# Performance work log

Measured on AMD Instinct MI355X. Metric: run time of the kernel, lower is better.

The kernel has to match this reference:

```python
import jax, jax.numpy as jnp
import numpy as np

LR = 0.1  # inner-loop learning rate from `param - 0.1 * grad`

D = 4096          # memory width d; key/val are (1, d) per docstring
CTX = 512         # loss_context_size: number of keys per update step


def setup_inputs() -> dict:
    key = jax.random.key(0)
    k1, k2, k3 = jax.random.split(key, 3)
    W = jax.random.normal(k1, (D, D), dtype=jnp.float32) / np.sqrt(D)
    keys = jax.random.normal(k2, (CTX, D), dtype=jnp.float32)
    vals = jax.random.normal(k3, (CTX, D), dtype=jnp.float32)
    return {"W": W, "keys": keys, "vals": vals}


def reference(W, keys, vals):
    # OneStep.forward: preds_i = functional_forward(key_i, (W,)) = key_i @ W,
    # loss = MSE(preds, vals); new_W = W - 0.1 * dloss/dW.
    # The per-key loop is batched into a single (CTX, D) x (D, D) matmul.
    def loss_fn(Wp):
        preds = keys @ Wp  # (CTX, D)
        return jnp.mean((preds - vals) ** 2)

    g = jax.grad(loss_fn)(W)
    return W - LR * g
```

## Files before the change

### kernel.cpp

```cpp
#include <hip/hip_runtime.h>
#include <hip/hip_bf16.h>


typedef __bf16 bf16_t;
typedef __bf16 bf16x8 __attribute__((ext_vector_type(8)));
typedef float f32x4 __attribute__((ext_vector_type(4)));

#define D_DIM 4096
#define CTX_N 512
#define UPD_SCALE 9.5367431640625e-8f

__device__ __forceinline__ void gld16(const bf16_t* g, bf16_t* l) {
    __builtin_amdgcn_global_load_lds(
        (const __attribute__((address_space(1))) void*)g,
        (__attribute__((address_space(3))) void*)l, 16, 0, 0);
}

__device__ __forceinline__ void t_body2(
    float* tile, const float* __restrict__ src, bf16_t* __restrict__ dstT,
    bf16_t* __restrict__ dstN, int M, int N, int bx, int by)
{
    const int tid = threadIdx.x;
    const int C0 = bx * 64, R0 = by * 64;
    const int r  = tid >> 2, cs = (tid & 3) * 16;

    const float* s = src + (size_t)(R0 + r) * N + C0 + cs;
    float f[16];
#pragma unroll
    for (int u = 0; u < 4; ++u) {
        const float4 v = ((const float4*)s)[u];
        f[4 * u + 0] = v.x; f[4 * u + 1] = v.y; f[4 * u + 2] = v.z; f[4 * u + 3] = v.w;
    }
#pragma unroll
    for (int u = 0; u < 16; ++u) tile[r * 65 + cs + u] = f[u];

    if (dstN) {
        bf16x8 v0, v1;
#pragma unroll
        for (int u = 0; u < 8; ++u) { v0[u] = (bf16_t)f[u]; v1[u] = (bf16_t)f[8 + u]; }
        bf16_t* d = dstN + (size_t)(R0 + r) * N + C0 + cs;
        *(bf16x8*)d = v0; *(bf16x8*)(d + 8) = v1;
    }
    __syncthreads();

    bf16x8 o0, o1;
#pragma unroll
    for (int u = 0; u < 8; ++u) {
        o0[u] = (bf16_t)tile[(cs + u) * 65 + r];
        o1[u] = (bf16_t)tile[(cs + 8 + u) * 65 + r];
    }
    bf16_t* d = dstT + (size_t)(C0 + r) * M + R0 + cs;
    *(bf16x8*)d = o0; *(bf16x8*)(d + 8) = o1;
}

__global__ __launch_bounds__(256) void t_all(
    const float* __restrict__ W, const float* __restrict__ K,
    const float* __restrict__ V, bf16_t* __restrict__ Wt,
    bf16_t* __restrict__ Kt, bf16_t* __restrict__ Kb, bf16_t* __restrict__ Vt)
{
    __shared__ float tile[64 * 65];
    const int y = blockIdx.y;
    if (y < 64)      t_body2(tile, W, Wt, nullptr, D_DIM, D_DIM, blockIdx.x, y);
    else if (y < 72) t_body2(tile, K, Kt, Kb,      CTX_N, D_DIM, blockIdx.x, y - 64);
    else             t_body2(tile, V, Vt, nullptr, CTX_N, D_DIM, blockIdx.x, y - 72);
}



__global__ __launch_bounds__(256, 2) void k1_residual(
    const bf16_t* __restrict__ Wt, const bf16_t* __restrict__ Kb,
    const bf16_t* __restrict__ Vt, bf16_t* __restrict__ Rt)
{
    __shared__ __align__(16) bf16_t stg[16384];

    const int tid = threadIdx.x, wave = tid >> 6, lane = tid & 63;
    const int j0 = blockIdx.x * 64, c0 = blockIdx.y * 64;
    const int l15 = lane & 15, quad = lane >> 4;
    const int wm = wave >> 1, wn = wave & 1;

    f32x4 acc[2][2] = {};

    const int rl = lane >> 3;
    const int sl = ((lane & 7) ^ rl) * 8;
    const bf16_t* gA0 = Wt + (size_t)(j0 + wave * 8      + rl) * D_DIM + sl;
    const bf16_t* gA1 = Wt + (size_t)(j0 + wave * 8 + 32 + rl) * D_DIM + sl;
    const bf16_t* gB0 = Kb + (size_t)(c0 + wave * 8      + rl) * D_DIM + sl;
    const bf16_t* gB1 = Kb + (size_t)(c0 + wave * 8 + 32 + rl) * D_DIM + sl;

    auto stage = [&](int bsel, int t) {
        bf16_t* buf = stg + bsel * 8192;
        gld16(gA0 + t * 64, buf + (size_t)wave * 512 + lane * 8);
        gld16(gA1 + t * 64, buf + (size_t)(wave + 4) * 512 + lane * 8);
        gld16(gB0 + t * 64, buf + 4096 + (size_t)wave * 512 + lane * 8);
        gld16(gB1 + t * 64, buf + 4096 + (size_t)(wave + 4) * 512 + lane * 8);
    };

#define K1_COMPUTE(BSEL)                                                     \
    {                                                                        \
        const bf16_t* buf = stg + (BSEL) * 8192;                             \
        const int r3 = l15 & 7, uh = l15 >> 3;                               \
        bf16x8 a[2][2], b[2][2];                                             \
        _Pragma("unroll")                                                    \
        for (int kk = 0; kk < 2; ++kk) {                                     \
            const int slot = r3 * 8 + ((kk * 4 + quad) ^ r3);                \
            _Pragma("unroll")                                                \
            for (int x = 0; x < 2; ++x) {                                    \
                const int uA = wm * 4 + x * 2 + uh;                          \
                const int uB = wn * 4 + x * 2 + uh;                          \
                a[x][kk] = *(const bf16x8*)(buf + uA * 512 + slot * 8);      \
                b[x][kk] = *(const bf16x8*)(buf + 4096 + uB * 512 + slot * 8); \
            }                                                                \
        }                                                                    \
        _Pragma("unroll")                                                    \
        for (int kk = 0; kk < 2; ++kk)                                       \
            _Pragma("unroll")                                                \
            for (int mi = 0; mi < 2; ++mi)                                   \
                _Pragma("unroll")                                            \
                for (int ni = 0; ni < 2; ++ni)                               \
                    acc[mi][ni] = __builtin_amdgcn_mfma_f32_16x16x32_bf16(   \
                        a[mi][kk], b[ni][kk], acc[mi][ni], 0, 0, 0);         \
    }

    stage(0, 0);
    __syncthreads();
#pragma unroll 1
    for (int t = 0; t < 62; t += 2) {
        stage(1, t + 1);
        __builtin_amdgcn_sched_barrier(0);
        K1_COMPUTE(0);
        __syncthreads();
        stage(0, t + 2);
        __builtin_amdgcn_sched_barrier(0);
        K1_COMPUTE(1);
        __syncthreads();
    }
    stage(1, 63);
    __builtin_amdgcn_sched_barrier(0);
    K1_COMPUTE(0);
    __syncthreads();
    K1_COMPUTE(1);

    {
        const size_t base =
            (size_t)(j0 + wm * 32 + quad * 4) * CTX_N + c0 + wn * 32 + l15;
#pragma unroll
        for (int mi = 0; mi < 2; ++mi)
#pragma unroll
            for (int r = 0; r < 4; ++r) {
                const size_t rowb = base + (size_t)(mi * 16 + r) * CTX_N;
#pragma unroll
                for (int ni = 0; ni < 2; ++ni) {
                    const size_t idx = rowb + ni * 16;
                    Rt[idx] = (bf16_t)(acc[mi][ni][r] - (float)Vt[idx]);
                }
            }
    }
}


#define K2_COMPUTE(BSEL)                                                      \
    {                                                                         \
        const bf16_t* bufA = stg + (BSEL) * 12288;                            \
        const bf16_t* bufB = bufA + 8192;                                     \
        const int sgx = (quad ^ (l15 & 3)) * 8;                               \
        bf16x8 af[4], bq[4];                                                  \
        _Pragma("unroll")                                                     \
        for (int mi = 0; mi < 4; ++mi)                                        \
            af[mi] = *(const bf16x8*)(                                        \
                bufA + ((wave >> 1) * 4 + mi) * 512 + l15 * 32 + sgx);        \
        _Pragma("unroll")                                                     \
        for (int ni = 0; ni < 4; ++ni)                                        \
            bq[ni] = *(const bf16x8*)(                                        \
                bufB + ((wave & 1) * 4 + ni) * 512 + l15 * 32 + sgx);         \
        _Pragma("unroll")                                                     \
        for (int mi = 0; mi < 4; ++mi)                                        \
            _Pragma("unroll")                                                 \
            for (int ni = 0; ni < 4; ++ni)                                    \
                acc[mi][ni] = __builtin_amdgcn_mfma_f32_16x16x32_bf16(        \
                    af[mi], bq[ni], acc[mi][ni], 0, 0, 0);                    \
    }

__global__ __launch_bounds__(512, 2) void k2_update(
    const bf16_t* __restrict__ Kt, const bf16_t* __restrict__ Rt,
    const float* __restrict__ W, float* __restrict__ out)
{
    __shared__ __align__(16) bf16_t stg[2 * 12288];

    const int tid = threadIdx.x;

    const int id = blockIdx.x + 32 * blockIdx.y;
    const int xp = (id >> 3) & 31;
    const int yp = (id & 7) + 8 * (id >> 8);
    const int j0 = xp * 128, i0 = yp * 256;

    const int lane = tid & 63, wave = tid >> 6;
    const int wi = (wave >> 1) * 64, wj = (wave & 1) * 64;
    const int l15 = lane & 15, quad = lane >> 4;

    f32x4 acc[4][4] = {};

    const int rl = lane >> 2;
    const int sl = ((lane & 3) ^ (rl & 3)) * 8;
    const bf16_t* gA0 = Kt + (size_t)(i0 + wave * 16       + rl) * CTX_N + sl;
    const bf16_t* gA1 = Kt + (size_t)(i0 + wave * 16 + 128 + rl) * CTX_N + sl;
    const bf16_t* gB0 = Rt + (size_t)(j0 + wave * 16       + rl) * CTX_N + sl;

    auto stage = [&](int bsel, int cc) {
        bf16_t* buf = stg + bsel * 12288;
        gld16(gA0 + cc, buf + (size_t)wave * 512 + lane * 8);
        gld16(gA1 + cc, buf + (size_t)(wave + 8) * 512 + lane * 8);
        gld16(gB0 + cc, buf + 8192 + (size_t)wave * 512 + lane * 8);
    };

    stage(0, 0);
    __syncthreads();
#pragma unroll 1
    for (int t = 1; t <= 13; t += 2) {
        stage(1, t * 32);
        __builtin_amdgcn_sched_barrier(0);
        K2_COMPUTE(0);
        __syncthreads();
        stage(0, (t + 1) * 32);
        __builtin_amdgcn_sched_barrier(0);
        K2_COMPUTE(1);
        __syncthreads();
    }
    stage(1, 15 * 32);
    __builtin_amdgcn_sched_barrier(0);
    K2_COMPUTE(0);
    __syncthreads();
    K2_COMPUTE(1);

    const size_t base = (size_t)(i0 + wi + quad * 4) * D_DIM + j0 + wj + l15;
    const float* wp = W + base;
    float*       op = out + base;

    float w0[16], w1[16];
#pragma unroll
    for (int r = 0; r < 4; ++r)
#pragma unroll
        for (int ni = 0; ni < 4; ++ni)
            w0[r * 4 + ni] = wp[(size_t)r * D_DIM + ni * 16];

#pragma unroll
    for (int mi = 0; mi < 4; ++mi) {
        float* wcur = (mi & 1) ? w1 : w0;
        float* wnxt = (mi & 1) ? w0 : w1;
        if (mi < 3) {
#pragma unroll
            for (int r = 0; r < 4; ++r)
#pragma unroll
                for (int ni = 0; ni < 4; ++ni)
                    wnxt[r * 4 + ni] =
                        wp[(size_t)((mi + 1) * 16 + r) * D_DIM + ni * 16];
        }
#pragma unroll
        for (int r = 0; r < 4; ++r)
#pragma unroll
            for (int ni = 0; ni < 4; ++ni)
                op[(size_t)(mi * 16 + r) * D_DIM + ni * 16] =
                    wcur[r * 4 + ni] - UPD_SCALE * acc[mi][ni][r];
    }
}

extern "C" void kernel_launch(void* const* d_in, const int* in_sizes, int n_in,
                              void* d_out, int out_size, void* d_ws, size_t ws_size,
                              hipStream_t stream) {
    const float* W = (const float*)d_in[0];
    const float* K = (const float*)d_in[1];
    const float* V = (const float*)d_in[2];
    float* out = (float*)d_out;

    char* ws = (char*)d_ws;
    bf16_t* Wt = (bf16_t*)(ws);
    bf16_t* Kt = (bf16_t*)(ws + (size_t)32 * 1024 * 1024);
    bf16_t* Kb = (bf16_t*)(ws + (size_t)36 * 1024 * 1024);
    bf16_t* Vt = (bf16_t*)(ws + (size_t)40 * 1024 * 1024);
    bf16_t* Rt = (bf16_t*)(ws + (size_t)44 * 1024 * 1024);

    t_all      <<<dim3(64, 80), 256, 0, stream>>>(W, K, V, Wt, Kt, Kb, Vt);
    k1_residual<<<dim3(64, 8),  256, 0, stream>>>(Wt, Kb, Vt, Rt);
    k2_update  <<<dim3(32, 16), 512, 0, stream>>>(Kt, Rt, W, out);
}
```

Measured before the change: 193.0 us.

## Split-K the residual GEMM with larger 128x128 tiles and a reduce kernel

The residual GEMM (keys @ W) now uses 128x128 output tiles with a 4x4 MFMA accumulator per wave and splits the K dimension into four 1024-wide chunks. Each chunk writes fp32 partial sums to workspace, and a new reduction kernel adds the four partials, subtracts V and writes the bf16 residual. The larger tiles improve data reuse per LDS load, and split-K keeps the grid at 512 blocks. The cost is an extra kernel launch, 32 MB of fp32 partial traffic written and read back, and double the LDS per block, which may reduce occupancy.

```diff
diff --git a/kernel.cpp b/kernel.cpp
--- a/kernel.cpp
+++ b/kernel.cpp
@@ -67,64 +67,73 @@
 
 
 
-__global__ __launch_bounds__(256, 2) void k1_residual(
+__global__ __launch_bounds__(256, 2) void k1_partial(
     const bf16_t* __restrict__ Wt, const bf16_t* __restrict__ Kb,
-    const bf16_t* __restrict__ Vt, bf16_t* __restrict__ Rt)
-{
-    __shared__ __align__(16) bf16_t stg[16384];
+    float* __restrict__ Rp)
+{
+    __shared__ __align__(16) bf16_t stg[2 * 16384];
 
     const int tid = threadIdx.x, wave = tid >> 6, lane = tid & 63;
-    const int j0 = blockIdx.x * 64, c0 = blockIdx.y * 64;
+    const int j0 = blockIdx.x * 128;
+    const int cb = blockIdx.y & 3, ks = blockIdx.y >> 2;
+    const int c0 = cb * 128;
+    const size_t k0 = (size_t)ks * 1024;
     const int l15 = lane & 15, quad = lane >> 4;
     const int wm = wave >> 1, wn = wave & 1;
 
-    f32x4 acc[2][2] = {};
+    f32x4 acc[4][4] = {};
 
     const int rl = lane >> 3;
     const int sl = ((lane & 7) ^ rl) * 8;
-    const bf16_t* gA0 = Wt + (size_t)(j0 + wave * 8      + rl) * D_DIM + sl;
-    const bf16_t* gA1 = Wt + (size_t)(j0 + wave * 8 + 32 + rl) * D_DIM + sl;
-    const bf16_t* gB0 = Kb + (size_t)(c0 + wave * 8      + rl) * D_DIM + sl;
-    const bf16_t* gB1 = Kb + (size_t)(c0 + wave * 8 + 32 + rl) * D_DIM + sl;
+
+    const bf16_t* gA[4];
+    const bf16_t* gB[4];
+#pragma unroll
+    for (int i = 0; i < 4; ++i) {
+        const int u = wave * 4 + i;
+        gA[i] = Wt + (size_t)(j0 + u * 8 + rl) * D_DIM + k0 + sl;
+        gB[i] = Kb + (size_t)(c0 + u * 8 + rl) * D_DIM + k0 + sl;
+    }
 
     auto stage = [&](int bsel, int t) {
-        bf16_t* buf = stg + bsel * 8192;
-        gld16(gA0 + t * 64, buf + (size_t)wave * 512 + lane * 8);
-        gld16(gA1 + t * 64, buf + (size_t)(wave + 4) * 512 + lane * 8);
-        gld16(gB0 + t * 64, buf + 4096 + (size_t)wave * 512 + lane * 8);
-        gld16(gB1 + t * 64, buf + 4096 + (size_t)(wave + 4) * 512 + lane * 8);
+        bf16_t* buf = stg + bsel * 16384;
+#pragma unroll
+        for (int i = 0; i < 4; ++i) {
+            const int u = wave * 4 + i;
+            gld16(gA[i] + t * 64, buf + (size_t)u * 512 + lane * 8);
+            gld16(gB[i] + t * 64, buf + 8192 + (size_t)u * 512 + lane * 8);
+        }
     };
 
 #define K1_COMPUTE(BSEL)                                                     \
     {                                                                        \
-        const bf16_t* buf = stg + (BSEL) * 8192;                             \
+        const bf16_t* buf = stg + (BSEL) * 16384;                            \
         const int r3 = l15 & 7, uh = l15 >> 3;                               \
-        bf16x8 a[2][2], b[2][2];                                             \
         _Pragma("unroll")                                                    \
         for (int kk = 0; kk < 2; ++kk) {                                     \
             const int slot = r3 * 8 + ((kk * 4 + quad) ^ r3);                \
+            bf16x8 af[4], bq[4];                                             \
             _Pragma("unroll")                                                \
-            for (int x = 0; x < 2; ++x) {                                    \
-                const int uA = wm * 4 + x * 2 + uh;                          \
-                const int uB = wn * 4 + x * 2 + uh;                          \
-                a[x][kk] = *(const bf16x8*)(buf + uA * 512 + slot * 8);      \
-                b[x][kk] = *(const bf16x8*)(buf + 4096 + uB * 512 + slot * 8); \
-            }                                                                \
+            for (int mi = 0; mi < 4; ++mi)                                   \
+                af[mi] = *(const bf16x8*)(                                   \
+                    buf + (wm * 8 + mi * 2 + uh) * 512 + slot * 8);          \
+            _Pragma("unroll")                                                \
+            for (int ni = 0; ni < 4; ++ni)                                   \
+                bq[ni] = *(const bf16x8*)(                                   \
+                    buf + 8192 + (wn * 8 + ni * 2 + uh) * 512 + slot * 8);   \
+            _Pragma("unroll")                                                \
+            for (int mi = 0; mi < 4; ++mi)                                   \
+                _Pragma("unroll")                                            \
+                for (int ni = 0; ni < 4; ++ni)                               \
+                    acc[mi][ni] = __builtin_amdgcn_mfma_f32_16x16x32_bf16(   \
+                        af[mi], bq[ni], acc[mi][ni], 0, 0, 0);               \
         }                                                                    \
-        _Pragma("unroll")                                                    \
-        for (int kk = 0; kk < 2; ++kk)                                       \
-            _Pragma("unroll")                                                \
-            for (int mi = 0; mi < 2; ++mi)                                   \
-                _Pragma("unroll")                                            \
-                for (int ni = 0; ni < 2; ++ni)                               \
-                    acc[mi][ni] = __builtin_amdgcn_mfma_f32_16x16x32_bf16(   \
-                        a[mi][kk], b[ni][kk], acc[mi][ni], 0, 0, 0);         \
     }
 
     stage(0, 0);
     __syncthreads();
 #pragma unroll 1
-    for (int t = 0; t < 62; t += 2) {
+    for (int t = 0; t < 14; t += 2) {
         stage(1, t + 1);
         __builtin_amdgcn_sched_barrier(0);
         K1_COMPUTE(0);
@@ -134,27 +143,50 @@
         K1_COMPUTE(1);
         __syncthreads();
     }
-    stage(1, 63);
+    stage(1, 15);
     __builtin_amdgcn_sched_barrier(0);
     K1_COMPUTE(0);
     __syncthreads();
     K1_COMPUTE(1);
 
     {
+        float* rp = Rp + (size_t)ks * D_DIM * CTX_N;
         const size_t base =
-            (size_t)(j0 + wm * 32 + quad * 4) * CTX_N + c0 + wn * 32 + l15;
-#pragma unroll
-        for (int mi = 0; mi < 2; ++mi)
+            (size_t)(j0 + wm * 64 + quad * 4) * CTX_N + c0 + wn * 64 + l15;
+#pragma unroll
+        for (int mi = 0; mi < 4; ++mi)
 #pragma unroll
             for (int r = 0; r < 4; ++r) {
                 const size_t rowb = base + (size_t)(mi * 16 + r) * CTX_N;
 #pragma unroll
-                for (int ni = 0; ni < 2; ++ni) {
-                    const size_t idx = rowb + ni * 16;
-                    Rt[idx] = (bf16_t)(acc[mi][ni][r] - (float)Vt[idx]);
-                }
+                for (int ni = 0; ni < 4; ++ni)
+                    rp[rowb + ni * 16] = acc[mi][ni][r];
             }
     }
+}
+
+__global__ __launch_bounds__(256) void k1_reduce(
+    const float* __restrict__ Rp, const bf16_t* __restrict__ Vt,
+    bf16_t* __restrict__ Rt)
+{
+    const size_t base = ((size_t)blockIdx.x * 256 + threadIdx.x) * 8;
+    const size_t slice = (size_t)D_DIM * CTX_N;
+
+    f32x4 s0 = {}, s1 = {};
+#pragma unroll
+    for (int ks = 0; ks < 4; ++ks) {
+        const f32x4 a = *(const f32x4*)(Rp + ks * slice + base);
+        const f32x4 b = *(const f32x4*)(Rp + ks * slice + base + 4);
+        s0 += a; s1 += b;
+    }
+    const bf16x8 vv = *(const bf16x8*)(Vt + base);
+    bf16x8 o;
+#pragma unroll
+    for (int j = 0; j < 4; ++j) {
+        o[j]     = (bf16_t)(s0[j] - (float)vv[j]);
+        o[4 + j] = (bf16_t)(s1[j] - (float)vv[4 + j]);
+    }
+    *(bf16x8*)(Rt + base) = o;
 }
 
 
@@ -277,8 +309,10 @@
     bf16_t* Kb = (bf16_t*)(ws + (size_t)36 * 1024 * 1024);
     bf16_t* Vt = (bf16_t*)(ws + (size_t)40 * 1024 * 1024);
     bf16_t* Rt = (bf16_t*)(ws + (size_t)44 * 1024 * 1024);
+    float*  Rp = (float*) (ws + (size_t)48 * 1024 * 1024);
 
     t_all      <<<dim3(64, 80), 256, 0, stream>>>(W, K, V, Wt, Kt, Kb, Vt);
-    k1_residual<<<dim3(64, 8),  256, 0, stream>>>(Wt, Kb, Vt, Rt);
+    k1_partial <<<dim3(32, 16), 256, 0, stream>>>(Wt, Kb, Rp);
+    k1_reduce  <<<dim3(1024),   256, 0, stream>>>(Rp, Vt, Rt);
     k2_update  <<<dim3(32, 16), 512, 0, stream>>>(Kt, Rt, W, out);
 }
```

New measurement: 194.0 us. No clear change (+0.5%).
